# Kernel optimization log

Measured on AMD Instinct MI355X. Metric: run time of the kernel, lower is better.

The kernel has to match this reference:

```python
import jax, jax.numpy as jnp
import numpy as np

C = 128            # in_channels
B, H, W = 4, 256, 256
WS = 8             # window_size
N = WS * WS        # tokens per window
HIDDEN = int(N ** 0.5) * 2   # WindowScoreBias hidden_dim = 16
NUM_HEADS = 2


def setup_inputs() -> dict:
    key = jax.random.key(0)
    ks = jax.random.split(key, 8)
    # deterministic relative-position table (mirrors _gen_window_score_bias_input, reduction=1)
    coords = np.stack(np.meshgrid(np.arange(WS), np.arange(WS), indexing='ij'), axis=2).reshape(N, 2)
    delta = (coords[:, None, :] - coords[None, :, :]).reshape(N * N, 2)
    uniq, index = np.unique(delta, axis=0, return_inverse=True)  # lexsorted unique == sorted tuples
    uniq = uniq.astype(np.float32) / np.abs(uniq).max()
    return {
        'x': jax.random.normal(ks[0], (B, C, H, W), jnp.float32),
        'delta': jnp.asarray(uniq),                       # [U, 2]
        'index': jnp.asarray(index.astype(np.int32)),     # [N*N]
        'w_qkv': jax.random.normal(ks[1], (3 * C, C), jnp.float32) * 0.02,
        'b_qkv': jnp.zeros((3 * C,), jnp.float32),
        'w_head': jax.random.normal(ks[2], (C, C), jnp.float32) * 0.02,
        'b_head': jnp.zeros((C,), jnp.float32),
        'w_b1': jax.random.normal(ks[3], (HIDDEN, 2), jnp.float32) * 0.02,
        'b_b1': jnp.zeros((HIDDEN,), jnp.float32),
        'w_b2': jax.random.normal(ks[4], (1, HIDDEN), jnp.float32) * 0.02,
        'b_b2': jnp.zeros((1,), jnp.float32),
        'w_c1': jax.random.normal(ks[5], (C, C, 1, 1), jnp.float32) * (2.0 / C) ** 0.5,
        'b_c1': jnp.zeros((C,), jnp.float32),
        'w_c2': jax.random.normal(ks[6], (C, C, 3, 3), jnp.float32) * (2.0 / (9 * C)) ** 0.5,
        'b_c2': jnp.zeros((C,), jnp.float32),
    }


def _conv(x, w, b):
    y = jax.lax.conv_general_dilated(x, w, (1, 1), 'VALID',
                                     dimension_numbers=('NCHW', 'OIHW', 'NCHW'))
    return y + b[None, :, None, None]


def reference(x, delta, index, w_qkv, b_qkv, w_head, b_head,
              w_b1, b_b1, w_b2, b_b2, w_c1, b_c1, w_c2, b_c2):
    Bx, Cx, Hx, Wx = x.shape
    oh, ow = Hx // WS, Wx // WS
    dk = Cx // NUM_HEADS
    # WindowScoreBias: MLP over unique deltas, gather by index -> [N, N]
    hmlp = jax.nn.gelu(delta @ w_b1.T + b_b1, approximate=False)
    bias = (hmlp @ w_b2.T + b_b2)[index].reshape(N, N)
    # window partition: BCHW -> (B*oh*ow, N, C)
    xw = x.reshape(Bx, Cx, oh, WS, ow, WS).transpose(0, 2, 4, 3, 5, 1).reshape(Bx * oh * ow, N, Cx)
    qkv = xw @ w_qkv.T + b_qkv
    q, k, v = jnp.split(qkv, 3, axis=-1)
    heads = lambda t: t.reshape(-1, N, NUM_HEADS, dk).transpose(0, 2, 1, 3)  # [Bw,h,N,dk]
    q, k, v = heads(q), heads(k), heads(v)
    scores = jnp.einsum('bhnd,bhmd->bhnm', q, k) * (1.0 / float(np.sqrt(dk))) + bias
    attn = jax.nn.softmax(scores, axis=-1)
    o = jnp.einsum('bhnm,bhmd->bhnd', attn, v)
    o = o.transpose(0, 2, 1, 3).reshape(-1, N, Cx) @ w_head.T + b_head
    # window reverse: (B*oh*ow, N, C) -> BCHW
    o = o.reshape(Bx, oh, ow, WS, WS, Cx).transpose(0, 5, 1, 3, 2, 4).reshape(Bx, Cx, Hx, Wx)
    x = x + o
    # conv_mlp: 1x1 conv -> GELU -> replication pad -> 3x3 conv -> LeakyReLU(0.1)
    y = jax.nn.gelu(_conv(x, w_c1, b_c1), approximate=False)
    y = jnp.pad(y, ((0, 0), (0, 0), (1, 1), (1, 1)), mode='edge')
    y = _conv(y, w_c2, b_c2)
    y = jnp.where(y > 0, y, 0.1 * y)
    return x + y
```

## Files before the change

kernel.cpp:

```cpp
#include <hip/hip_runtime.h>

typedef short v8s __attribute__((ext_vector_type(8)));
typedef float v4f __attribute__((ext_vector_type(4)));
typedef unsigned short v4u __attribute__((ext_vector_type(4)));

#define MFMA(a,b,c) __builtin_amdgcn_mfma_f32_16x16x32_bf16((a),(b),(c),0,0,0)

__device__ __forceinline__ unsigned short f2b(float f) {
  unsigned int x = __builtin_bit_cast(unsigned int, f);
  x += 0x7fffu + ((x >> 16) & 1u);
  return (unsigned short)(x >> 16);
}

__device__ __forceinline__ float b2f(unsigned short u) {
  unsigned int x = ((unsigned int)u) << 16;
  return __builtin_bit_cast(float, x);
}

__device__ __forceinline__ float gelu_exact(float v) {
  return 0.5f * v * (1.0f + erff(v * 0.70710678118654752f));
}

__global__ void prep_kernel(const float* __restrict__ wqkv, const float* __restrict__ whead,
                            const float* __restrict__ wc1, const float* __restrict__ wc2,
                            const float* __restrict__ delta, const int* __restrict__ indexv,
                            const float* __restrict__ wb1, const float* __restrict__ bb1,
                            const float* __restrict__ wb2, const float* __restrict__ bb2,
                            unsigned short* __restrict__ wqkv_b, unsigned short* __restrict__ whead_b,
                            unsigned short* __restrict__ wc1_b, unsigned short* __restrict__ w2r_b,
                            float* __restrict__ bias_ws) {
  int i = blockIdx.x * 256 + threadIdx.x;
  if (i < 49152) { wqkv_b[i] = f2b(wqkv[i]); return; }
  i -= 49152;
  if (i < 16384) { whead_b[i] = f2b(whead[i]); return; }
  i -= 16384;
  if (i < 16384) { wc1_b[i] = f2b(wc1[i]); return; }
  i -= 16384;
  if (i < 147456) {
    int o = i / 1152; int rem = i - o * 1152; int pos = rem >> 7; int c = rem & 127;
    w2r_b[i] = f2b(wc2[o * 1152 + c * 9 + pos]);
    return;
  }
  i -= 147456;
  if (i < 4096) {
    int u = indexv[i];
    float d0 = delta[2 * u], d1 = delta[2 * u + 1];
    float acc = bb2[0];
    #pragma unroll
    for (int j = 0; j < 16; ++j) {
      float t = d0 * wb1[2 * j] + d1 * wb1[2 * j + 1] + bb1[j];
      acc += gelu_exact(t) * wb2[j];
    }
    bias_ws[i] = acc;
  }
}

__global__ __launch_bounds__(256, 3) void attn_kernel(
    const float* __restrict__ x, const float* __restrict__ bias,
    const unsigned short* __restrict__ wqkv_b, const unsigned short* __restrict__ whead_b,
    const unsigned short* __restrict__ wc1_b,
    const float* __restrict__ bqkv, const float* __restrict__ bhead, const float* __restrict__ bc1,
    unsigned short* __restrict__ x1h, unsigned short* __restrict__ ybuf) {
  __shared__ unsigned short U0[128 * 72];
  __shared__ unsigned short QP[64 * 136];
  __shared__ unsigned short KO[64 * 136];
  unsigned short* const XS = U0;
  unsigned short* const VT = U0;

  const int tid = threadIdx.x;
  const int wv = tid >> 6, lane = tid & 63, quad = lane >> 4, l15 = lane & 15;
  const int bid0 = blockIdx.x;
  const int bid = ((bid0 & 7) << 9) | (bid0 >> 3);
  const int bb = bid >> 10, rem = bid & 1023;
  const int h0 = (rem >> 5) * 8, w0 = (rem & 31) * 8;
  const float* xwin = x + (size_t)bb * 128 * 65536 + h0 * 256 + w0;

  #pragma unroll
  for (int it = 0; it < 4; ++it) {
    int idx = it * 256 + tid;
    int c = idx >> 3, py = idx & 7;
    const float* p = xwin + c * 65536 + py * 256;
    float4 a0 = *(const float4*)p;
    float4 a1 = *(const float4*)(p + 4);
    float av[8] = {a0.x, a0.y, a0.z, a0.w, a1.x, a1.y, a1.z, a1.w};
    int base = (py * 8) * 136 + c;
    #pragma unroll
    for (int j = 0; j < 8; ++j) XS[base + j * 136] = f2b(av[j]);
  }
  __syncthreads();

  v4u vpk[2][4];
  #pragma unroll
  for (int part = 0; part < 3; ++part) {
    v4f acc[2][4] = {};
    #pragma unroll
    for (int ks = 0; ks < 4; ++ks) {
      v8s afr[2];
      #pragma unroll
      for (int i = 0; i < 2; ++i)
        afr[i] = *(const v8s*)(wqkv_b + (size_t)(part * 128 + (2 * wv + i) * 16 + l15) * 128 + ks * 32 + quad * 8);
      v8s bfr[4];
      #pragma unroll
      for (int ct = 0; ct < 4; ++ct)
        bfr[ct] = *(const v8s*)(&XS[(ct * 16 + l15) * 136 + ks * 32 + quad * 8]);
      #pragma unroll
      for (int i = 0; i < 2; ++i)
        #pragma unroll
        for (int ct = 0; ct < 4; ++ct)
          acc[i][ct] = MFMA(afr[i], bfr[ct], acc[i][ct]);
    }
    #pragma unroll
    for (int i = 0; i < 2; ++i) {
      int ol0 = (2 * wv + i) * 16 + quad * 4;
      float4 bq = *(const float4*)(bqkv + part * 128 + ol0);
      float bqa[4] = {bq.x, bq.y, bq.z, bq.w};
      #pragma unroll
      for (int ct = 0; ct < 4; ++ct) {
        int token = ct * 16 + l15;
        v4u pk = {f2b(acc[i][ct][0] + bqa[0]), f2b(acc[i][ct][1] + bqa[1]),
                  f2b(acc[i][ct][2] + bqa[2]), f2b(acc[i][ct][3] + bqa[3])};
        if (part == 0)      *(v4u*)(&QP[token * 136 + ol0]) = pk;
        else if (part == 1) *(v4u*)(&KO[token * 136 + ol0]) = pk;
        else                vpk[i][ct] = pk;
      }
    }
  }
  __syncthreads();

  #pragma unroll
  for (int i = 0; i < 2; ++i) {
    int ol0 = (2 * wv + i) * 16 + quad * 4;
    #pragma unroll
    for (int ct = 0; ct < 4; ++ct) {
      int token = ct * 16 + l15;
      VT[(ol0 + 0) * 72 + token] = vpk[i][ct][0];
      VT[(ol0 + 1) * 72 + token] = vpk[i][ct][1];
      VT[(ol0 + 2) * 72 + token] = vpk[i][ct][2];
      VT[(ol0 + 3) * 72 + token] = vpk[i][ct][3];
    }
  }

  const int t0 = wv * 16;
  v4f sc[2][4] = {};
  #pragma unroll
  for (int h = 0; h < 2; ++h)
    #pragma unroll
    for (int ks = 0; ks < 2; ++ks) {
      v8s afr = *(const v8s*)(&QP[(t0 + l15) * 136 + h * 64 + ks * 32 + quad * 8]);
      #pragma unroll
      for (int ct = 0; ct < 4; ++ct) {
        v8s bfr = *(const v8s*)(&KO[(ct * 16 + l15) * 136 + h * 64 + ks * 32 + quad * 8]);
        sc[h][ct] = MFMA(afr, bfr, sc[h][ct]);
      }
    }
  float linv[2][4];
  const int rowbase = (t0 + quad * 4) * 64 + l15;
  #pragma unroll
  for (int h = 0; h < 2; ++h) {
    float sv[4][4];
    #pragma unroll
    for (int ct = 0; ct < 4; ++ct)
      #pragma unroll
      for (int r = 0; r < 4; ++r)
        sv[ct][r] = sc[h][ct][r] * 0.125f + bias[rowbase + r * 64 + ct * 16];
    #pragma unroll
    for (int r = 0; r < 4; ++r) {
      float m = fmaxf(fmaxf(sv[0][r], sv[1][r]), fmaxf(sv[2][r], sv[3][r]));
      m = fmaxf(m, __shfl_xor(m, 1, 16));
      m = fmaxf(m, __shfl_xor(m, 2, 16));
      m = fmaxf(m, __shfl_xor(m, 4, 16));
      m = fmaxf(m, __shfl_xor(m, 8, 16));
      float s = 0.f;
      #pragma unroll
      for (int ct = 0; ct < 4; ++ct) { float p = __expf(sv[ct][r] - m); sv[ct][r] = p; s += p; }
      s += __shfl_xor(s, 1, 16);
      s += __shfl_xor(s, 2, 16);
      s += __shfl_xor(s, 4, 16);
      s += __shfl_xor(s, 8, 16);
      linv[h][r] = 1.0f / s;
    }
    #pragma unroll
    for (int ct = 0; ct < 4; ++ct)
      #pragma unroll
      for (int r = 0; r < 4; ++r)
        QP[(t0 + quad * 4 + r) * 136 + h * 64 + ct * 16 + l15] = f2b(sv[ct][r]);
  }
  __syncthreads();

  v4f ov[2][4] = {};
  #pragma unroll
  for (int h = 0; h < 2; ++h)
    #pragma unroll
    for (int ks = 0; ks < 2; ++ks) {
      v8s afr = *(const v8s*)(&QP[(t0 + l15) * 136 + h * 64 + ks * 32 + quad * 8]);
      #pragma unroll
      for (int ct = 0; ct < 4; ++ct) {
        v8s bfr = *(const v8s*)(&VT[(h * 64 + ct * 16 + l15) * 72 + ks * 32 + quad * 8]);
        ov[h][ct] = MFMA(afr, bfr, ov[h][ct]);
      }
    }
  #pragma unroll
  for (int h = 0; h < 2; ++h)
    #pragma unroll
    for (int ct = 0; ct < 4; ++ct)
      #pragma unroll
      for (int r = 0; r < 4; ++r)
        KO[(t0 + quad * 4 + r) * 136 + h * 64 + ct * 16 + l15] = f2b(ov[h][ct][r] * linv[h][r]);
  __syncthreads();

  v4f pj[8] = {};
  #pragma unroll
  for (int ks = 0; ks < 4; ++ks) {
    v8s afr = *(const v8s*)(&KO[(t0 + l15) * 136 + ks * 32 + quad * 8]);
    #pragma unroll
    for (int ct = 0; ct < 8; ++ct) {
      v8s bfr = *(const v8s*)(whead_b + (size_t)(ct * 16 + l15) * 128 + ks * 32 + quad * 8);
      pj[ct] = MFMA(afr, bfr, pj[ct]);
    }
  }
  {
    int token0 = t0 + quad * 4;
    int py = token0 >> 3, px = token0 & 7;
    #pragma unroll
    for (int ct = 0; ct < 8; ++ct) {
      int o = ct * 16 + l15;
      const float* xp = xwin + o * 65536 + py * 256 + px;
      float4 xi = *(const float4*)xp;
      float xa[4] = {xi.x, xi.y, xi.z, xi.w};
      float bh = bhead[o];
      #pragma unroll
      for (int r = 0; r < 4; ++r) XS[(token0 + r) * 136 + o] = f2b(xa[r] + pj[ct][r] + bh);
    }
  }
  __syncthreads();

  #pragma unroll
  for (int it = 0; it < 4; ++it) {
    int idx = it * 256 + tid;
    int token = idx >> 4, c8 = idx & 15;
    int py = token >> 3, px = token & 7;
    *(v8s*)(x1h + (size_t)((bb * 256 + h0 + py) * 256 + w0 + px) * 128 + c8 * 8) =
        *(const v8s*)(&XS[token * 136 + c8 * 8]);
  }

  v4f c1[2][4] = {};
  #pragma unroll
  for (int ks = 0; ks < 4; ++ks) {
    v8s afr[2];
    #pragma unroll
    for (int i = 0; i < 2; ++i)
      afr[i] = *(const v8s*)(wc1_b + (size_t)((2 * wv + i) * 16 + l15) * 128 + ks * 32 + quad * 8);
    v8s bfr[4];
    #pragma unroll
    for (int ct = 0; ct < 4; ++ct)
      bfr[ct] = *(const v8s*)(&XS[(ct * 16 + l15) * 136 + ks * 32 + quad * 8]);
    #pragma unroll
    for (int i = 0; i < 2; ++i)
      #pragma unroll
      for (int ct = 0; ct < 4; ++ct)
        c1[i][ct] = MFMA(afr[i], bfr[ct], c1[i][ct]);
  }
  #pragma unroll
  for (int i = 0; i < 2; ++i) {
    int o0 = (2 * wv + i) * 16 + quad * 4;
    float4 bc = *(const float4*)(bc1 + o0);
    float bca[4] = {bc.x, bc.y, bc.z, bc.w};
    #pragma unroll
    for (int ct = 0; ct < 4; ++ct) {
      int pix = ct * 16 + l15, ppy = pix >> 3, ppx = pix & 7;
      unsigned short g[4];
      #pragma unroll
      for (int r = 0; r < 4; ++r) g[r] = f2b(gelu_exact(c1[i][ct][r] + bca[r]));
      v4u pk = {g[0], g[1], g[2], g[3]};
      *(v4u*)(ybuf + (size_t)((bb * 256 + h0 + ppy) * 256 + w0 + ppx) * 128 + o0) = pk;
    }
  }
}

__global__ __launch_bounds__(256, 4) void conv2_kernel(
    const unsigned short* __restrict__ w2r, const unsigned short* __restrict__ ybuf,
    const unsigned short* __restrict__ x1h, const float* __restrict__ bc2, float* __restrict__ xo) {
  __shared__ unsigned short HALO[136 * 136];
  const int tid = threadIdx.x;
  const int wv = tid >> 6, lane = tid & 63, quad = lane >> 4, l15 = lane & 15;
  const int bid0 = blockIdx.x;
  const int bid = ((bid0 & 7) << 9) | (bid0 >> 3);
  const int bb = bid >> 10, rem = bid & 1023;
  const int y0 = (rem >> 3) * 2, x0 = (rem & 7) * 32;

  v4u xpre[2][4];
  #pragma unroll
  for (int i = 0; i < 2; ++i) {
    int o0 = (2 * wv + i) * 16 + quad * 4;
    #pragma unroll
    for (int ct = 0; ct < 4; ++ct) {
      int pix = ct * 16 + l15, typ = pix >> 5, txp = pix & 31;
      xpre[i][ct] = *(const v4u*)(x1h + (size_t)((bb * 256 + y0 + typ) * 256 + x0 + txp) * 128 + o0);
    }
  }

  for (int it = 0; it < 9; ++it) {
    int idx = it * 256 + tid;
    if (idx < 2176) {
      int hp = idx >> 4, c8 = idx & 15;
      int iy = hp / 34, ix = hp - iy * 34;
      int hy = y0 - 1 + iy; hy = hy < 0 ? 0 : (hy > 255 ? 255 : hy);
      int hx = x0 - 1 + ix; hx = hx < 0 ? 0 : (hx > 255 ? 255 : hx);
      *(v8s*)(&HALO[hp * 136 + c8 * 8]) =
          *(const v8s*)(ybuf + (size_t)((bb * 256 + hy) * 256 + hx) * 128 + c8 * 8);
    }
  }
  __syncthreads();

  v4f acc[2][4] = {};
  int bct[4];
  #pragma unroll
  for (int ct = 0; ct < 4; ++ct) {
    int pix = ct * 16 + l15, typ = pix >> 5, txp = pix & 31;
    bct[ct] = (typ * 34 + txp) * 136 + quad * 8;
  }
  const unsigned short* wb0 = w2r + (size_t)((2 * wv + 0) * 16 + l15) * 1152 + quad * 8;
  const unsigned short* wb1 = w2r + (size_t)((2 * wv + 1) * 16 + l15) * 1152 + quad * 8;
  #pragma unroll
  for (int ks = 0; ks < 36; ++ks) {
    const int pos = ks >> 2, cb = ks & 3;
    const int ky = pos / 3, kx = pos - ky * 3;
    const int koff = (ky * 34 + kx) * 136 + cb * 32;
    v8s a0 = *(const v8s*)(wb0 + ks * 32);
    v8s a1 = *(const v8s*)(wb1 + ks * 32);
    #pragma unroll
    for (int ct = 0; ct < 4; ++ct) {
      v8s bfr = *(const v8s*)(&HALO[bct[ct] + koff]);
      acc[0][ct] = MFMA(a0, bfr, acc[0][ct]);
      acc[1][ct] = MFMA(a1, bfr, acc[1][ct]);
    }
  }

  #pragma unroll
  for (int i = 0; i < 2; ++i) {
    int o0 = (2 * wv + i) * 16 + quad * 4;
    float4 bc = *(const float4*)(bc2 + o0);
    float bca[4] = {bc.x, bc.y, bc.z, bc.w};
    #pragma unroll
    for (int ct = 0; ct < 4; ++ct) {
      int pix = ct * 16 + l15, typ = pix >> 5, txp = pix & 31;
      float* po = xo + (size_t)(bb * 128 + o0) * 65536 + (y0 + typ) * 256 + (x0 + txp);
      #pragma unroll
      for (int r = 0; r < 4; ++r) {
        float v = acc[i][ct][r] + bca[r];
        v = v > 0.f ? v : 0.1f * v;
        po[(size_t)r * 65536] = v + b2f(xpre[i][ct][r]);
      }
    }
  }
}

extern "C" void kernel_launch(void* const* d_in, const int* in_sizes, int n_in,
                              void* d_out, int out_size, void* d_ws, size_t ws_size,
                              hipStream_t stream) {
  (void)in_sizes; (void)n_in; (void)out_size; (void)ws_size;
  const float* x      = (const float*)d_in[0];
  const float* delta  = (const float*)d_in[1];
  const int*   indexv = (const int*)d_in[2];
  const float* w_qkv  = (const float*)d_in[3];
  const float* b_qkv  = (const float*)d_in[4];
  const float* w_head = (const float*)d_in[5];
  const float* b_head = (const float*)d_in[6];
  const float* w_b1   = (const float*)d_in[7];
  const float* b_b1   = (const float*)d_in[8];
  const float* w_b2   = (const float*)d_in[9];
  const float* b_b2   = (const float*)d_in[10];
  const float* w_c1   = (const float*)d_in[11];
  const float* b_c1   = (const float*)d_in[12];
  const float* w_c2   = (const float*)d_in[13];
  const float* b_c2   = (const float*)d_in[14];
  float* out = (float*)d_out;

  char* ws = (char*)d_ws;
  float*          bias_ws = (float*)(ws + 0);
  unsigned short* wqkv_b  = (unsigned short*)(ws + 16384);
  unsigned short* whead_b = (unsigned short*)(ws + 114688);
  unsigned short* wc1_b   = (unsigned short*)(ws + 147456);
  unsigned short* w2r_b   = (unsigned short*)(ws + 180224);
  unsigned short* ybuf    = (unsigned short*)(ws + 475136);
  unsigned short* x1h     = (unsigned short*)(ws + 475136 + 67108864);

  prep_kernel<<<912, 256, 0, stream>>>(w_qkv, w_head, w_c1, w_c2, delta, indexv,
                                       w_b1, b_b1, w_b2, b_b2,
                                       wqkv_b, whead_b, wc1_b, w2r_b, bias_ws);
  attn_kernel<<<4096, 256, 0, stream>>>(x, bias_ws, wqkv_b, whead_b, wc1_b,
                                        b_qkv, b_head, b_c1, x1h, ybuf);
  conv2_kernel<<<4096, 256, 0, stream>>>(w2r_b, ybuf, x1h, b_c2, out);
}
```

Before: 702.8 us.

## Write conv2 output as fp16 NHWC in place, transpose to NCHW in separate kernel

conv2 now writes its residual-added result in fp16 channel-last layout back into the x1 buffer, which also switches from bf16 to fp16. A new transpose kernel then converts it through shared memory to the fp32 NCHW output with coalesced stores. This is meant to replace the strided 4-byte scattered NCHW stores in conv2. The cost is an extra kernel launch, an extra pass that reads and writes the full tensor, and fp16 rounding of the final output.

```diff
diff --git a/kernel.cpp b/kernel.cpp
--- a/kernel.cpp
+++ b/kernel.cpp
@@ -3,6 +3,8 @@
 typedef short v8s __attribute__((ext_vector_type(8)));
 typedef float v4f __attribute__((ext_vector_type(4)));
 typedef unsigned short v4u __attribute__((ext_vector_type(4)));
+typedef _Float16 h4 __attribute__((ext_vector_type(4)));
+typedef _Float16 h8 __attribute__((ext_vector_type(8)));
 
 #define MFMA(a,b,c) __builtin_amdgcn_mfma_f32_16x16x32_bf16((a),(b),(c),0,0,0)
 
@@ -60,7 +62,7 @@
     const unsigned short* __restrict__ wqkv_b, const unsigned short* __restrict__ whead_b,
     const unsigned short* __restrict__ wc1_b,
     const float* __restrict__ bqkv, const float* __restrict__ bhead, const float* __restrict__ bc1,
-    unsigned short* __restrict__ x1h, unsigned short* __restrict__ ybuf) {
+    _Float16* __restrict__ t16, unsigned short* __restrict__ ybuf) {
   __shared__ unsigned short U0[128 * 72];
   __shared__ unsigned short QP[64 * 136];
   __shared__ unsigned short KO[64 * 136];
@@ -239,8 +241,11 @@
     int idx = it * 256 + tid;
     int token = idx >> 4, c8 = idx & 15;
     int py = token >> 3, px = token & 7;
-    *(v8s*)(x1h + (size_t)((bb * 256 + h0 + py) * 256 + w0 + px) * 128 + c8 * 8) =
-        *(const v8s*)(&XS[token * 136 + c8 * 8]);
+    v8s d = *(const v8s*)(&XS[token * 136 + c8 * 8]);
+    h8 o;
+    #pragma unroll
+    for (int j = 0; j < 8; ++j) o[j] = (_Float16)b2f((unsigned short)d[j]);
+    *(h8*)(t16 + (size_t)((bb * 256 + h0 + py) * 256 + w0 + px) * 128 + c8 * 8) = o;
   }
 
   v4f c1[2][4] = {};
@@ -279,7 +284,7 @@
 
 __global__ __launch_bounds__(256, 4) void conv2_kernel(
     const unsigned short* __restrict__ w2r, const unsigned short* __restrict__ ybuf,
-    const unsigned short* __restrict__ x1h, const float* __restrict__ bc2, float* __restrict__ xo) {
+    _Float16* __restrict__ t16, const float* __restrict__ bc2) {
   __shared__ unsigned short HALO[136 * 136];
   const int tid = threadIdx.x;
   const int wv = tid >> 6, lane = tid & 63, quad = lane >> 4, l15 = lane & 15;
@@ -288,14 +293,14 @@
   const int bb = bid >> 10, rem = bid & 1023;
   const int y0 = (rem >> 3) * 2, x0 = (rem & 7) * 32;
 
-  v4u xpre[2][4];
+  h4 xpre[2][4];
   #pragma unroll
   for (int i = 0; i < 2; ++i) {
     int o0 = (2 * wv + i) * 16 + quad * 4;
     #pragma unroll
     for (int ct = 0; ct < 4; ++ct) {
       int pix = ct * 16 + l15, typ = pix >> 5, txp = pix & 31;
-      xpre[i][ct] = *(const v4u*)(x1h + (size_t)((bb * 256 + y0 + typ) * 256 + x0 + txp) * 128 + o0);
+      xpre[i][ct] = *(const h4*)(t16 + (size_t)((bb * 256 + y0 + typ) * 256 + x0 + txp) * 128 + o0);
     }
   }
 
@@ -344,14 +349,43 @@
     #pragma unroll
     for (int ct = 0; ct < 4; ++ct) {
       int pix = ct * 16 + l15, typ = pix >> 5, txp = pix & 31;
-      float* po = xo + (size_t)(bb * 128 + o0) * 65536 + (y0 + typ) * 256 + (x0 + txp);
+      h4 hv;
       #pragma unroll
       for (int r = 0; r < 4; ++r) {
         float v = acc[i][ct][r] + bca[r];
         v = v > 0.f ? v : 0.1f * v;
-        po[(size_t)r * 65536] = v + b2f(xpre[i][ct][r]);
+        hv[r] = (_Float16)(v + (float)xpre[i][ct][r]);
       }
-    }
+      *(h4*)(t16 + (size_t)((bb * 256 + y0 + typ) * 256 + x0 + txp) * 128 + o0) = hv;
+    }
+  }
+}
+
+__global__ __launch_bounds__(256, 2) void tr_kernel(
+    const _Float16* __restrict__ t16, float* __restrict__ xo) {
+  __shared__ _Float16 T[128 * 257];
+  const int tid = threadIdx.x;
+  const int bid = blockIdx.x;
+  const int b = bid >> 8, h = bid & 255;
+  const _Float16* src = t16 + (size_t)((b * 256 + h) * 256) * 128;
+
+  #pragma unroll
+  for (int it = 0; it < 16; ++it) {
+    int idx = it * 256 + tid;
+    int px = idx >> 4, c8 = idx & 15;
+    h8 v = *(const h8*)(src + px * 128 + c8 * 8);
+    #pragma unroll
+    for (int j = 0; j < 8; ++j) T[(c8 * 8 + j) * 257 + px] = v[j];
+  }
+  __syncthreads();
+
+  const int wv = tid >> 6, lane = tid & 63;
+  #pragma unroll
+  for (int cc = 0; cc < 32; ++cc) {
+    int c = wv * 32 + cc;
+    const _Float16* t = &T[c * 257 + lane * 4];
+    float4 o = make_float4((float)t[0], (float)t[1], (float)t[2], (float)t[3]);
+    *(float4*)(xo + (size_t)(b * 128 + c) * 65536 + h * 256 + lane * 4) = o;
   }
 }
 
@@ -383,12 +417,13 @@
   unsigned short* wc1_b   = (unsigned short*)(ws + 147456);
   unsigned short* w2r_b   = (unsigned short*)(ws + 180224);
   unsigned short* ybuf    = (unsigned short*)(ws + 475136);
-  unsigned short* x1h     = (unsigned short*)(ws + 475136 + 67108864);
+  _Float16*       t16     = (_Float16*)(ws + 475136 + 67108864);
 
   prep_kernel<<<912, 256, 0, stream>>>(w_qkv, w_head, w_c1, w_c2, delta, indexv,
                                        w_b1, b_b1, w_b2, b_b2,
                                        wqkv_b, whead_b, wc1_b, w2r_b, bias_ws);
   attn_kernel<<<4096, 256, 0, stream>>>(x, bias_ws, wqkv_b, whead_b, wc1_b,
-                                        b_qkv, b_head, b_c1, x1h, ybuf);
-  conv2_kernel<<<4096, 256, 0, stream>>>(w2r_b, ybuf, x1h, b_c2, out);
-}
+                                        b_qkv, b_head, b_c1, t16, ybuf);
+  conv2_kernel<<<4096, 256, 0, stream>>>(w2r_b, ybuf, t16, b_c2);
+  tr_kernel<<<1024, 256, 0, stream>>>(t16, out);
+}
```

Result: slower. 717.8 us (+2.1%).

## Pre-transpose input to NHWC bf16 in a separate kernel before attention

Applied to the files above, without the earlier changes.

Adds a kernel that transposes the NCHW fp32 input into an NHWC bf16 buffer through shared memory. The attention kernel then loads window tiles with contiguous 16-byte vector reads instead of strided per-channel fp32 loads, and reads the residual from the same buffer, which it overwrites in place with x1. This targets the strided, poorly coalesced global reads in the attention kernel, at the cost of an extra launch and a full read and write pass. The residual is now taken from bf16 rather than fp32, so precision drops slightly.

```diff
diff --git a/kernel.cpp b/kernel.cpp
--- a/kernel.cpp
+++ b/kernel.cpp
@@ -55,12 +55,46 @@
   }
 }
 
+__global__ __launch_bounds__(256, 2) void xt_kernel(
+    const float* __restrict__ x, unsigned short* __restrict__ t16) {
+  __shared__ unsigned short T[256 * 129];
+  const int tid = threadIdx.x;
+  const int bid = blockIdx.x;
+  const int b = bid >> 8, h = bid & 255;
+  const float* src = x + (size_t)b * 128 * 65536 + h * 256;
+
+  #pragma unroll
+  for (int it = 0; it < 32; ++it) {
+    int u = it * 256 + tid;
+    int c = u >> 6, w4 = u & 63;
+    float4 v = *(const float4*)(src + (size_t)c * 65536 + w4 * 4);
+    int base = (w4 * 4) * 129 + c;
+    T[base]       = f2b(v.x);
+    T[base + 129] = f2b(v.y);
+    T[base + 258] = f2b(v.z);
+    T[base + 387] = f2b(v.w);
+  }
+  __syncthreads();
+
+  unsigned short* dst = t16 + (size_t)((b * 256 + h) * 256) * 128;
+  #pragma unroll
+  for (int it = 0; it < 16; ++it) {
+    int idx = it * 256 + tid;
+    int px = idx >> 4, c8 = idx & 15;
+    const unsigned short* t = &T[px * 129 + c8 * 8];
+    v8s o;
+    #pragma unroll
+    for (int j = 0; j < 8; ++j) o[j] = (short)t[j];
+    *(v8s*)(dst + px * 128 + c8 * 8) = o;
+  }
+}
+
 __global__ __launch_bounds__(256, 3) void attn_kernel(
-    const float* __restrict__ x, const float* __restrict__ bias,
+    const float* __restrict__ bias,
     const unsigned short* __restrict__ wqkv_b, const unsigned short* __restrict__ whead_b,
     const unsigned short* __restrict__ wc1_b,
     const float* __restrict__ bqkv, const float* __restrict__ bhead, const float* __restrict__ bc1,
-    unsigned short* __restrict__ x1h, unsigned short* __restrict__ ybuf) {
+    unsigned short* __restrict__ t16, unsigned short* __restrict__ ybuf) {
   __shared__ unsigned short U0[128 * 72];
   __shared__ unsigned short QP[64 * 136];
   __shared__ unsigned short KO[64 * 136];
@@ -73,19 +107,14 @@
   const int bid = ((bid0 & 7) << 9) | (bid0 >> 3);
   const int bb = bid >> 10, rem = bid & 1023;
   const int h0 = (rem >> 5) * 8, w0 = (rem & 31) * 8;
-  const float* xwin = x + (size_t)bb * 128 * 65536 + h0 * 256 + w0;
 
   #pragma unroll
   for (int it = 0; it < 4; ++it) {
     int idx = it * 256 + tid;
-    int c = idx >> 3, py = idx & 7;
-    const float* p = xwin + c * 65536 + py * 256;
-    float4 a0 = *(const float4*)p;
-    float4 a1 = *(const float4*)(p + 4);
-    float av[8] = {a0.x, a0.y, a0.z, a0.w, a1.x, a1.y, a1.z, a1.w};
-    int base = (py * 8) * 136 + c;
-    #pragma unroll
-    for (int j = 0; j < 8; ++j) XS[base + j * 136] = f2b(av[j]);
+    int token = idx >> 4, c8 = idx & 15;
+    int py = token >> 3, px = token & 7;
+    *(v8s*)(&XS[token * 136 + c8 * 8]) =
+        *(const v8s*)(t16 + (size_t)((bb * 256 + h0 + py) * 256 + w0 + px) * 128 + c8 * 8);
   }
   __syncthreads();
 
@@ -221,15 +250,16 @@
   {
     int token0 = t0 + quad * 4;
     int py = token0 >> 3, px = token0 & 7;
+    const unsigned short* xtw = t16 + (size_t)((bb * 256 + h0 + py) * 256 + w0 + px) * 128;
     #pragma unroll
     for (int ct = 0; ct < 8; ++ct) {
       int o = ct * 16 + l15;
-      const float* xp = xwin + o * 65536 + py * 256 + px;
-      float4 xi = *(const float4*)xp;
-      float xa[4] = {xi.x, xi.y, xi.z, xi.w};
       float bh = bhead[o];
       #pragma unroll
-      for (int r = 0; r < 4; ++r) XS[(token0 + r) * 136 + o] = f2b(xa[r] + pj[ct][r] + bh);
+      for (int r = 0; r < 4; ++r) {
+        float xa = b2f(xtw[(size_t)r * 128 + o]);
+        XS[(token0 + r) * 136 + o] = f2b(xa + pj[ct][r] + bh);
+      }
     }
   }
   __syncthreads();
@@ -239,7 +269,7 @@
     int idx = it * 256 + tid;
     int token = idx >> 4, c8 = idx & 15;
     int py = token >> 3, px = token & 7;
-    *(v8s*)(x1h + (size_t)((bb * 256 + h0 + py) * 256 + w0 + px) * 128 + c8 * 8) =
+    *(v8s*)(t16 + (size_t)((bb * 256 + h0 + py) * 256 + w0 + px) * 128 + c8 * 8) =
         *(const v8s*)(&XS[token * 136 + c8 * 8]);
   }
 
@@ -279,7 +309,7 @@
 
 __global__ __launch_bounds__(256, 4) void conv2_kernel(
     const unsigned short* __restrict__ w2r, const unsigned short* __restrict__ ybuf,
-    const unsigned short* __restrict__ x1h, const float* __restrict__ bc2, float* __restrict__ xo) {
+    const unsigned short* __restrict__ t16, const float* __restrict__ bc2, float* __restrict__ xo) {
   __shared__ unsigned short HALO[136 * 136];
   const int tid = threadIdx.x;
   const int wv = tid >> 6, lane = tid & 63, quad = lane >> 4, l15 = lane & 15;
@@ -295,7 +325,7 @@
     #pragma unroll
     for (int ct = 0; ct < 4; ++ct) {
       int pix = ct * 16 + l15, typ = pix >> 5, txp = pix & 31;
-      xpre[i][ct] = *(const v4u*)(x1h + (size_t)((bb * 256 + y0 + typ) * 256 + x0 + txp) * 128 + o0);
+      xpre[i][ct] = *(const v4u*)(t16 + (size_t)((bb * 256 + y0 + typ) * 256 + x0 + txp) * 128 + o0);
     }
   }
 
@@ -383,12 +413,13 @@
   unsigned short* wc1_b   = (unsigned short*)(ws + 147456);
   unsigned short* w2r_b   = (unsigned short*)(ws + 180224);
   unsigned short* ybuf    = (unsigned short*)(ws + 475136);
-  unsigned short* x1h     = (unsigned short*)(ws + 475136 + 67108864);
+  unsigned short* t16     = (unsigned short*)(ws + 475136 + 67108864);
 
   prep_kernel<<<912, 256, 0, stream>>>(w_qkv, w_head, w_c1, w_c2, delta, indexv,
                                        w_b1, b_b1, w_b2, b_b2,
                                        wqkv_b, whead_b, wc1_b, w2r_b, bias_ws);
-  attn_kernel<<<4096, 256, 0, stream>>>(x, bias_ws, wqkv_b, whead_b, wc1_b,
-                                        b_qkv, b_head, b_c1, x1h, ybuf);
-  conv2_kernel<<<4096, 256, 0, stream>>>(w2r_b, ybuf, x1h, b_c2, out);
-}
+  xt_kernel<<<1024, 256, 0, stream>>>(x, t16);
+  attn_kernel<<<4096, 256, 0, stream>>>(bias_ws, wqkv_b, whead_b, wc1_b,
+                                        b_qkv, b_head, b_c1, t16, ybuf);
+  conv2_kernel<<<4096, 256, 0, stream>>>(w2r_b, ybuf, t16, b_c2, out);
+}
```

Result: no change. 693.1 us (-1.4%).
